# Optimization experiments

Hardware: AMD Instinct MI355X
Metric: run time of the kernel (lower is better)

The kernel has to match this reference:

```python
import jax, jax.numpy as jnp
import numpy as np

EMB = 768
N_HEADS = 12
HEAD_DIM = EMB // N_HEADS


def setup_inputs() -> dict:
    key = jax.random.key(0)
    k_x, k_w1, k_b1, k_w2, k_b2 = jax.random.split(key, 5)
    B, T = 8, 1024
    s = 0.02
    return {
        "x": jax.random.normal(k_x, (B, T, EMB), dtype=jnp.float32),
        "w_attn": jax.random.normal(k_w1, (EMB, 3 * EMB), dtype=jnp.float32) * s,
        "b_attn": jax.random.normal(k_b1, (3 * EMB,), dtype=jnp.float32) * s,
        "w_proj": jax.random.normal(k_w2, (EMB, EMB), dtype=jnp.float32) * s,
        "b_proj": jax.random.normal(k_b2, (EMB,), dtype=jnp.float32) * s,
    }


def reference(x, w_attn, b_attn, w_proj, b_proj):
    B, T, C = x.shape
    qkv = x @ w_attn + b_attn                       # [B,T,3C]
    q, k, v = jnp.split(qkv, 3, axis=2)
    # [B,T,C] -> [B,H,T,D]
    q = q.reshape(B, T, N_HEADS, HEAD_DIM).transpose(0, 2, 1, 3)
    k = k.reshape(B, T, N_HEADS, HEAD_DIM).transpose(0, 2, 1, 3)
    v = v.reshape(B, T, N_HEADS, HEAD_DIM).transpose(0, 2, 1, 3)
    scale = HEAD_DIM ** -0.5
    att = jnp.einsum("bhqd,bhkd->bhqk", q, k) * scale  # [B,H,T,T]
    causal = jnp.tril(jnp.ones((T, T), dtype=bool))
    att = jnp.where(causal, att, -jnp.inf)
    att = jax.nn.softmax(att, axis=-1)
    out = jnp.einsum("bhqk,bhkd->bhqd", att, v)        # [B,H,T,D]
    out = out.transpose(0, 2, 1, 3).reshape(B, T, C)
    return out @ w_proj + b_proj
```

## Files before the change

kernel.cpp:

```cpp
#include <hip/hip_runtime.h>
#include <hip/hip_bf16.h>
#include <math.h>

#define BATCH 8
#define SEQ   1024
#define EMB   768
#define NH    12
#define HD    64
#define QKVW  (3 * EMB)
#define VOFF  (2 * EMB)

typedef short short8   __attribute__((ext_vector_type(8)));
typedef float floatx4  __attribute__((ext_vector_type(4)));

__device__ __forceinline__ short f2bf(float f) {
    union { float f; unsigned u; } v; v.f = f;
    unsigned r = (v.u + 0x7fffu + ((v.u >> 16) & 1u)) >> 16;
    return (short)r;
}

__device__ __forceinline__ void async_load16(const void* g, void* l) {
    __builtin_amdgcn_global_load_lds(
        (const __attribute__((address_space(1))) unsigned int*)g,
        (__attribute__((address_space(3))) unsigned int*)l, 16, 0, 0);
}

__global__ __launch_bounds__(256) void cvt_bf16(
    const float* __restrict__ in, short* __restrict__ out, int n8)
{
    const int i = blockIdx.x * 256 + threadIdx.x;
    if (i >= n8) return;
    const float4 a = ((const float4*)in)[2 * i];
    const float4 b = ((const float4*)in)[2 * i + 1];
    short8 s;
    s[0] = f2bf(a.x); s[1] = f2bf(a.y); s[2] = f2bf(a.z); s[3] = f2bf(a.w);
    s[4] = f2bf(b.x); s[5] = f2bf(b.y); s[6] = f2bf(b.z); s[7] = f2bf(b.w);
    ((short8*)out)[i] = s;
}

__global__ __launch_bounds__(256) void transpose_to_bf16(
    const float* __restrict__ in, short* __restrict__ outT, int R, int C)
{
    __shared__ float t[32][33];
    const int c0 = blockIdx.x * 32, r0 = blockIdx.y * 32;
    const int lx = threadIdx.x & 31, ly = threadIdx.x >> 5;
    #pragma unroll
    for (int i = 0; i < 32; i += 8)
        t[ly + i][lx] = in[(size_t)(r0 + ly + i) * C + c0 + lx];
    __syncthreads();
    #pragma unroll
    for (int i = 0; i < 32; i += 8)
        outT[(size_t)(c0 + ly + i) * R + r0 + lx] = f2bf(t[lx][ly + i]);
}

#define GBK 32

template <int MODE>
__global__ __launch_bounds__(256) void gemm_bf16(
    const short* __restrict__ A, const short* __restrict__ Bt,
    const float* __restrict__ bias, void* __restrict__ Cout,
    short* __restrict__ vt, int M, int N, int K)
{
    __shared__ __align__(16) short As[128 * GBK];
    __shared__ __align__(16) short Bs[128 * GBK];

    const int tid  = threadIdx.x;
    const int wave = tid >> 6;
    const int lane = tid & 63;
    const int ln15 = lane & 15;
    const int quad = lane >> 4;
    const int wr   = (wave >> 1) * 64;
    const int wc   = (wave & 1) * 64;
    const int row0 = blockIdx.y * 128;
    const int col0 = blockIdx.x * 128;

    floatx4 acc[4][4];
    #pragma unroll
    for (int i = 0; i < 4; ++i)
        #pragma unroll
        for (int j = 0; j < 4; ++j) acc[i][j] = (floatx4){0.f, 0.f, 0.f, 0.f};

    for (int k0 = 0; k0 < K; k0 += GBK) {
        __syncthreads();
        #pragma unroll
        for (int half = 0; half < 2; ++half) {
            const int r  = half * 64 + wave * 16 + (lane >> 2);
            const int kk = (lane & 3) * 8;
            async_load16(A  + (size_t)(row0 + r) * K + k0 + kk,
                         &As[(half * 64 + wave * 16) * GBK + lane * 8]);
            async_load16(Bt + (size_t)(col0 + r) * K + k0 + kk,
                         &Bs[(half * 64 + wave * 16) * GBK + lane * 8]);
        }
        __syncthreads();

        short8 af[4], bf[4];
        #pragma unroll
        for (int t = 0; t < 4; ++t)
            af[t] = *(const short8*)&As[(wr + t * 16 + ln15) * GBK + quad * 8];
        #pragma unroll
        for (int t = 0; t < 4; ++t)
            bf[t] = *(const short8*)&Bs[(wc + t * 16 + ln15) * GBK + quad * 8];
        #pragma unroll
        for (int i = 0; i < 4; ++i)
            #pragma unroll
            for (int j = 0; j < 4; ++j)
                acc[i][j] = __builtin_amdgcn_mfma_f32_16x16x32_bf16(af[i], bf[j], acc[i][j], 0, 0, 0);
    }

    if (MODE == 1 && col0 >= VOFF) {
        #pragma unroll
        for (int i = 0; i < 4; ++i)
            #pragma unroll
            for (int reg = 0; reg < 4; ++reg) {
                const int r = row0 + wr + i * 16 + quad * 4 + reg;
                #pragma unroll
                for (int j = 0; j < 4; ++j) {
                    const int c  = col0 + wc + j * 16 + ln15;
                    const int c2 = c - VOFF;
                    const float v = acc[i][j][reg] + bias[c];
                    vt[(size_t)(r >> 10) * (EMB * SEQ) + (size_t)c2 * SEQ + (r & 1023)] = f2bf(v);
                }
            }
    } else {
        #pragma unroll
        for (int i = 0; i < 4; ++i)
            #pragma unroll
            for (int reg = 0; reg < 4; ++reg) {
                const int r = row0 + wr + i * 16 + quad * 4 + reg;
                #pragma unroll
                for (int j = 0; j < 4; ++j) {
                    const int c = col0 + wc + j * 16 + ln15;
                    const float v = acc[i][j][reg] + bias[c];
                    if (MODE == 1) ((short*)Cout)[(size_t)r * N + c] = f2bf(v);
                    else           ((float*)Cout)[(size_t)r * N + c] = v;
                }
            }
    }
}

#define LDK 72

__global__ __launch_bounds__(256) void attn_mfma(
    const short* __restrict__ qkv, const short* __restrict__ vt,
    short* __restrict__ out)
{
    __shared__ __align__(16) short Ks[64 * LDK];
    __shared__ __align__(16) short Vt[64 * LDK];
    __shared__ __align__(16) short Ps[4 * 16 * LDK];

    const int tid  = threadIdx.x;
    const int wave = tid >> 6;
    const int lane = tid & 63;
    const int ln15 = lane & 15;
    const int quad = lane >> 4;

    const int qc = 15 - (int)(blockIdx.x / (BATCH * NH));
    const int bh = blockIdx.x % (BATCH * NH);
    const int h  = bh % NH;
    const int b  = bh / NH;

    const int q0w = qc * 64 + wave * 16;

    const short* qkv_b = qkv + (size_t)b * SEQ * QKVW + h * HD;
    const short* Kg  = qkv_b + EMB;
    const short* Vtg = vt + ((size_t)b * EMB + h * HD) * SEQ;

    short8 qf[2];
    {
        const short* qrow = qkv_b + (size_t)(q0w + ln15) * QKVW;
        qf[0] = *(const short8*)(qrow + quad * 8);
        qf[1] = *(const short8*)(qrow + quad * 8 + 32);
    }

    floatx4 o[4];
    #pragma unroll
    for (int i = 0; i < 4; ++i) o[i] = (floatx4){0.f, 0.f, 0.f, 0.f};
    float lp[4] = {0.f, 0.f, 0.f, 0.f};

    const int rr = tid >> 3;
    const int c8 = (tid & 7) * 8;

    for (int kt = 0; kt <= qc; ++kt) {
        #pragma unroll
        for (int p = 0; p < 2; ++p) {
            const int r2 = rr + p * 32;
            *(uint4*)&Ks[r2 * LDK + c8] =
                *(const uint4*)(Kg + (size_t)(kt * 64 + r2) * QKVW + c8);
            *(uint4*)&Vt[r2 * LDK + c8] =
                *(const uint4*)(Vtg + (size_t)r2 * SEQ + kt * 64 + c8);
        }
        __syncthreads();

        floatx4 s[4];
        #pragma unroll
        for (int i = 0; i < 4; ++i) s[i] = (floatx4){0.f, 0.f, 0.f, 0.f};
        #pragma unroll
        for (int st = 0; st < 2; ++st)
            #pragma unroll
            for (int sub = 0; sub < 4; ++sub) {
                const short8 kf = *(const short8*)&Ks[(ln15 + sub * 16) * LDK + quad * 8 + st * 32];
                s[sub] = __builtin_amdgcn_mfma_f32_16x16x32_bf16(qf[st], kf, s[sub], 0, 0, 0);
            }

        const bool diag = (kt == qc);
        #pragma unroll
        for (int sub = 0; sub < 4; ++sub)
            #pragma unroll
            for (int reg = 0; reg < 4; ++reg) {
                float pv = __expf(s[sub][reg] * 0.125f);
                if (diag && (ln15 + sub * 16 > wave * 16 + quad * 4 + reg)) pv = 0.f;
                s[sub][reg] = pv;
            }
        #pragma unroll
        for (int reg = 0; reg < 4; ++reg)
            lp[reg] += (s[0][reg] + s[1][reg]) + (s[2][reg] + s[3][reg]);

        short* Pw = &Ps[wave * 16 * LDK];
        #pragma unroll
        for (int sub = 0; sub < 4; ++sub)
            #pragma unroll
            for (int reg = 0; reg < 4; ++reg) {
                const int qr   = quad * 4 + reg;
                const int kr8  = sub * 2 + (ln15 >> 3);
                const int slot = (kr8 + 5 * quad + reg) & 7;
                Pw[qr * LDK + slot * 8 + (ln15 & 7)] = f2bf(s[sub][reg]);
            }

        short8 pf[2];
        #pragma unroll
        for (int st = 0; st < 2; ++st) {
            const int slot = ((quad + 4 * st) + 5 * (ln15 >> 2) + (ln15 & 3)) & 7;
            pf[st] = *(const short8*)&Pw[ln15 * LDK + slot * 8];
        }

        #pragma unroll
        for (int st = 0; st < 2; ++st)
            #pragma unroll
            for (int sub = 0; sub < 4; ++sub) {
                const short8 vf = *(const short8*)&Vt[(ln15 + sub * 16) * LDK + quad * 8 + st * 32];
                o[sub] = __builtin_amdgcn_mfma_f32_16x16x32_bf16(pf[st], vf, o[sub], 0, 0, 0);
            }

        __syncthreads();
    }

    #pragma unroll
    for (int reg = 0; reg < 4; ++reg) {
        float t = lp[reg];
        #pragma unroll
        for (int off = 1; off <= 8; off <<= 1)
            t += __shfl_xor(t, off, 64);
        const float inv = 1.0f / t;
        const size_t row = (size_t)(b * SEQ + q0w + quad * 4 + reg) * EMB + h * HD;
        #pragma unroll
        for (int sub = 0; sub < 4; ++sub)
            out[row + ln15 + sub * 16] = f2bf(o[sub][reg] * inv);
    }
}

extern "C" void kernel_launch(void* const* d_in, const int* in_sizes, int n_in,
                              void* d_out, int out_size, void* d_ws, size_t ws_size,
                              hipStream_t stream)
{
    const float* x      = (const float*)d_in[0];
    const float* w_attn = (const float*)d_in[1];
    const float* b_attn = (const float*)d_in[2];
    const float* w_proj = (const float*)d_in[3];
    const float* b_proj = (const float*)d_in[4];
    float* out = (float*)d_out;

    const int M = BATCH * SEQ;

    short* xb    = (short*)d_ws;
    short* waT   = xb    + (size_t)M * EMB;
    short* wpT   = waT   + (size_t)QKVW * EMB;
    short* qkvb  = wpT   + (size_t)EMB * EMB;
    short* vtb   = qkvb  + (size_t)M * QKVW;
    short* attnb = vtb   + (size_t)BATCH * EMB * SEQ;

    dim3 blk(256);

    cvt_bf16<<<dim3((M * EMB) / 8 / 256), blk, 0, stream>>>(x, xb, (M * EMB) / 8);
    transpose_to_bf16<<<dim3(QKVW / 32, EMB / 32), blk, 0, stream>>>(w_attn, waT, EMB, QKVW);
    transpose_to_bf16<<<dim3(EMB / 32, EMB / 32), blk, 0, stream>>>(w_proj, wpT, EMB, EMB);

    gemm_bf16<1><<<dim3(QKVW / 128, M / 128), blk, 0, stream>>>(
        xb, waT, b_attn, qkvb, vtb, M, QKVW, EMB);

    attn_mfma<<<dim3(16 * BATCH * NH), blk, 0, stream>>>(qkvb, vtb, attnb);

    gemm_bf16<0><<<dim3(EMB / 128, M / 128), blk, 0, stream>>>(
        attnb, wpT, b_proj, out, nullptr, M, EMB, EMB);
}
```

Measured before the change: 220.2 us.

## Double GEMM K-tile, XOR-swizzle LDS, and vectorize epilogue stores via operand swap

```diff
diff --git a/kernel.cpp b/kernel.cpp
--- a/kernel.cpp
+++ b/kernel.cpp
@@ -53,7 +53,7 @@
         outT[(size_t)(c0 + ly + i) * R + r0 + lx] = f2bf(t[lx][ly + i]);
 }
 
-#define GBK 32
+#define GBK 64
 
 template <int MODE>
 __global__ __launch_bounds__(256) void gemm_bf16(
@@ -74,6 +74,8 @@
     const int row0 = blockIdx.y * 128;
     const int col0 = blockIdx.x * 128;
 
+    const bool trans = (MODE == 0) || (col0 < VOFF);
+
     floatx4 acc[4][4];
     #pragma unroll
     for (int i = 0; i < 4; ++i)
@@ -83,58 +85,85 @@
     for (int k0 = 0; k0 < K; k0 += GBK) {
         __syncthreads();
         #pragma unroll
+        for (int p = 0; p < 4; ++p) {
+            const int id  = p * 256 + tid;
+            const int row = id >> 3;
+            const int c   = (id & 7) ^ (row & 7);
+            async_load16(A  + (size_t)(row0 + row) * K + k0 + c * 8, &As[id * 8]);
+            async_load16(Bt + (size_t)(col0 + row) * K + k0 + c * 8, &Bs[id * 8]);
+        }
+        __syncthreads();
+
+        #pragma unroll
         for (int half = 0; half < 2; ++half) {
-            const int r  = half * 64 + wave * 16 + (lane >> 2);
-            const int kk = (lane & 3) * 8;
-            async_load16(A  + (size_t)(row0 + r) * K + k0 + kk,
-                         &As[(half * 64 + wave * 16) * GBK + lane * 8]);
-            async_load16(Bt + (size_t)(col0 + r) * K + k0 + kk,
-                         &Bs[(half * 64 + wave * 16) * GBK + lane * 8]);
-        }
-        __syncthreads();
-
-        short8 af[4], bf[4];
-        #pragma unroll
-        for (int t = 0; t < 4; ++t)
-            af[t] = *(const short8*)&As[(wr + t * 16 + ln15) * GBK + quad * 8];
-        #pragma unroll
-        for (int t = 0; t < 4; ++t)
-            bf[t] = *(const short8*)&Bs[(wc + t * 16 + ln15) * GBK + quad * 8];
-        #pragma unroll
-        for (int i = 0; i < 4; ++i)
-            #pragma unroll
-            for (int j = 0; j < 4; ++j)
-                acc[i][j] = __builtin_amdgcn_mfma_f32_16x16x32_bf16(af[i], bf[j], acc[i][j], 0, 0, 0);
-    }
-
-    if (MODE == 1 && col0 >= VOFF) {
-        #pragma unroll
-        for (int i = 0; i < 4; ++i)
-            #pragma unroll
-            for (int reg = 0; reg < 4; ++reg) {
-                const int r = row0 + wr + i * 16 + quad * 4 + reg;
+            short8 af[4], bf[4];
+            #pragma unroll
+            for (int t = 0; t < 4; ++t) {
+                const int ch = ((quad + half * 4) ^ (ln15 & 7)) * 8;
+                af[t] = *(const short8*)&As[(wr + t * 16 + ln15) * GBK + ch];
+                bf[t] = *(const short8*)&Bs[(wc + t * 16 + ln15) * GBK + ch];
+            }
+            if (trans) {
                 #pragma unroll
-                for (int j = 0; j < 4; ++j) {
-                    const int c  = col0 + wc + j * 16 + ln15;
-                    const int c2 = c - VOFF;
-                    const float v = acc[i][j][reg] + bias[c];
-                    vt[(size_t)(r >> 10) * (EMB * SEQ) + (size_t)c2 * SEQ + (r & 1023)] = f2bf(v);
+                for (int i = 0; i < 4; ++i)
+                    #pragma unroll
+                    for (int j = 0; j < 4; ++j)
+                        acc[i][j] = __builtin_amdgcn_mfma_f32_16x16x32_bf16(bf[j], af[i], acc[i][j], 0, 0, 0);
+            } else {
+                #pragma unroll
+                for (int i = 0; i < 4; ++i)
+                    #pragma unroll
+                    for (int j = 0; j < 4; ++j)
+                        acc[i][j] = __builtin_amdgcn_mfma_f32_16x16x32_bf16(af[i], bf[j], acc[i][j], 0, 0, 0);
+            }
+        }
+    }
+
+    if (MODE == 1 && !trans) {
+        #pragma unroll
+        for (int j = 0; j < 4; ++j) {
+            const int c  = col0 + wc + j * 16 + ln15;
+            const float bv = bias[c];
+            const int c2 = c - VOFF;
+            #pragma unroll
+            for (int i = 0; i < 4; ++i) {
+                const int r = row0 + wr + i * 16 + quad * 4;
+                union { short s[4]; unsigned long long u; } pk;
+                #pragma unroll
+                for (int reg = 0; reg < 4; ++reg)
+                    pk.s[reg] = f2bf(acc[i][j][reg] + bv);
+                *(unsigned long long*)&vt[(size_t)(r >> 10) * (EMB * SEQ) +
+                                          (size_t)c2 * SEQ + (r & 1023)] = pk.u;
+            }
+        }
+    } else {
+        float4 b4[4];
+        #pragma unroll
+        for (int j = 0; j < 4; ++j)
+            b4[j] = *(const float4*)&bias[col0 + wc + j * 16 + quad * 4];
+        #pragma unroll
+        for (int i = 0; i < 4; ++i) {
+            const int r = row0 + wr + i * 16 + ln15;
+            #pragma unroll
+            for (int j = 0; j < 4; ++j) {
+                const int c = col0 + wc + j * 16 + quad * 4;
+                if (MODE == 1) {
+                    union { short s[4]; unsigned long long u; } pk;
+                    pk.s[0] = f2bf(acc[i][j][0] + b4[j].x);
+                    pk.s[1] = f2bf(acc[i][j][1] + b4[j].y);
+                    pk.s[2] = f2bf(acc[i][j][2] + b4[j].z);
+                    pk.s[3] = f2bf(acc[i][j][3] + b4[j].w);
+                    *(unsigned long long*)&((short*)Cout)[(size_t)r * N + c] = pk.u;
+                } else {
+                    float4 v;
+                    v.x = acc[i][j][0] + b4[j].x;
+                    v.y = acc[i][j][1] + b4[j].y;
+                    v.z = acc[i][j][2] + b4[j].z;
+                    v.w = acc[i][j][3] + b4[j].w;
+                    *(float4*)&((float*)Cout)[(size_t)r * N + c] = v;
                 }
             }
-    } else {
-        #pragma unroll
-        for (int i = 0; i < 4; ++i)
-            #pragma unroll
-            for (int reg = 0; reg < 4; ++reg) {
-                const int r = row0 + wr + i * 16 + quad * 4 + reg;
-                #pragma unroll
-                for (int j = 0; j < 4; ++j) {
-                    const int c = col0 + wc + j * 16 + ln15;
-                    const float v = acc[i][j][reg] + bias[c];
-                    if (MODE == 1) ((short*)Cout)[(size_t)r * N + c] = f2bf(v);
-                    else           ((float*)Cout)[(size_t)r * N + c] = v;
-                }
-            }
+        }
     }
 }
 
```

New measurement: 217.6 us. About the same (-1.2%).
